# Optimization experiments

Measured on AMD Instinct MI355X. Metric: run time of the kernel, lower is better.

## Reference

```python
import jax, jax.numpy as jnp
import numpy as np

DIM = 1024
SCALE_DIM = 4
QK_DIM = DIM // SCALE_DIM  # 256
B, S = 4, 4096


def setup_inputs() -> dict:
    key = jax.random.key(0)
    ks = jax.random.split(key, 8)
    std = 1.0 / np.sqrt(DIM)  # keep activations O(1)
    return {
        "q": jax.random.normal(ks[0], (B, S, DIM), jnp.float32),
        "k": jax.random.normal(ks[1], (B, S, DIM), jnp.float32),
        "v": jax.random.normal(ks[2], (B, S, DIM), jnp.float32),
        "Wq": jax.random.normal(ks[3], (QK_DIM, DIM), jnp.float32) * std,
        "bq": jnp.zeros((QK_DIM,), jnp.float32),
        "Wk": jax.random.normal(ks[4], (QK_DIM, DIM), jnp.float32) * std,
        "bk": jnp.zeros((QK_DIM,), jnp.float32),
        "Wv": jax.random.normal(ks[5], (DIM, DIM), jnp.float32) * std,
        "bv": jnp.zeros((DIM,), jnp.float32),
    }


def reference(q, k, v, Wq, bq, Wk, bk, Wv, bv):
    scale = jnp.asarray(np.sqrt(QK_DIM), q.dtype)
    qp = jnp.einsum("bsd,ed->bse", q, Wq) + bq  # [B,S,QK_DIM]
    kp = jnp.einsum("bsd,ed->bse", k, Wk) + bk  # [B,S,QK_DIM]
    vp = jnp.einsum("bsd,ed->bse", v, Wv) + bv  # [B,S,DIM]
    z = jnp.einsum("bqe,bke->bqk", qp, kp)      # [B,S,S]
    z = jax.nn.sigmoid(z / scale)
    return jnp.einsum("bqk,bkd->bqd", z, vp)     # [B,S,DIM]
```

## Files before the change

### kernel.cpp

```cpp
#include <hip/hip_runtime.h>
#include <cstdint>
#include <cstddef>


typedef __bf16 bf16;
typedef __bf16 v8bf __attribute__((ext_vector_type(8)));
typedef __bf16 v4bf __attribute__((ext_vector_type(4)));
typedef float  v16f __attribute__((ext_vector_type(16)));

#define DIMV  1024
#define QKD   256
#define BATCH 4
#define SEQ   4096

#define TM 128
#define TN 128
#define BK 32

__global__ __launch_bounds__(256) void cast_f32_bf16(const float* __restrict__ in,
                                                     bf16* __restrict__ out, int n4) {
  int i = blockIdx.x * 256 + threadIdx.x;
  if (i >= n4) return;
  const float4 v = reinterpret_cast<const float4*>(in)[i];
  v4bf o;
  o[0] = (bf16)v.x; o[1] = (bf16)v.y; o[2] = (bf16)v.z; o[3] = (bf16)v.w;
  reinterpret_cast<v4bf*>(out)[i] = o;
}

__device__ __forceinline__ void gload_lds16(const void* g, void* l) {
  __builtin_amdgcn_global_load_lds((const __attribute__((address_space(1))) void*)g,
                                   (__attribute__((address_space(3))) void*)l,
                                   16, 0, 0);
}

template <int MODE>
__global__ __launch_bounds__(256) void gemm_nt(
    const bf16* __restrict__ A, long As_z,
    const bf16* __restrict__ B, long Bs_z,
    const float* __restrict__ bias0, const float* __restrict__ bias1,
    void* __restrict__ Cv, long Cs_z,
    int K, int lda, int ldb, int ldc) {
  __shared__ __align__(16) bf16 As[TM * BK];
  __shared__ __align__(16) bf16 Bs[TN * BK];
  const int tid  = threadIdx.x;
  const int wave = tid >> 6;
  const int lane = tid & 63;
  const int zb   = blockIdx.z;
  A = A + (size_t)zb * As_z;
  B = B + (size_t)zb * Bs_z;
  const float* bias = (MODE == 0 && zb) ? bias1 : bias0;

  const int row0 = blockIdx.x * TM;
  const int col0 = blockIdx.y * TN;
  const int wm = (wave & 1) * 64;
  const int wn = (wave >> 1) * 64;
  const int l31  = lane & 31;
  const int half = lane >> 5;

  v16f acc[2][2] = {};

  const char* gA = (const char*)A;
  const char* gB = (const char*)B;
  const size_t sA = (size_t)lda * 2;
  const size_t sB = (size_t)ldb * 2;

  const int row_s = tid >> 2;
  const int qg    = (tid & 3) ^ ((row_s >> 1) & 3);
  const int kb    = qg * 16;
  char* ldsA = (char*)As + wave * 1024;
  char* ldsB = (char*)Bs + wave * 1024;

  const char* pa0 = gA + (size_t)(row0 + row_s) * sA + kb;
  const char* pa1 = gA + (size_t)(row0 + row_s + 64) * sA + kb;
  const char* pb0 = gB + (size_t)(col0 + row_s) * sB + kb;
  const char* pb1 = gB + (size_t)(col0 + row_s + 64) * sB + kb;

  const int swz  = (lane >> 1) & 3;
  const int off0 = (half ^ swz) * 8;
  const int off1 = off0 ^ 16;
  const int raA0 = (wm + l31) * BK,      raA1 = (wm + 32 + l31) * BK;
  const int raB0 = (wn + l31) * BK,      raB1 = (wn + 32 + l31) * BK;

  const int kIters = K / BK;
  for (int kt = 0; kt < kIters; ++kt) {
    gload_lds16(pa0, ldsA);
    gload_lds16(pa1, ldsA + 4096);
    gload_lds16(pb0, ldsB);
    gload_lds16(pb1, ldsB + 4096);
    pa0 += BK * 2; pa1 += BK * 2; pb0 += BK * 2; pb1 += BK * 2;
    __syncthreads();

    v8bf a[2][2], b[2][2];
    a[0][0] = *(const v8bf*)&As[raA0 + off0];
    a[0][1] = *(const v8bf*)&As[raA0 + off1];
    a[1][0] = *(const v8bf*)&As[raA1 + off0];
    a[1][1] = *(const v8bf*)&As[raA1 + off1];
    b[0][0] = *(const v8bf*)&Bs[raB0 + off0];
    b[0][1] = *(const v8bf*)&Bs[raB0 + off1];
    b[1][0] = *(const v8bf*)&Bs[raB1 + off0];
    b[1][1] = *(const v8bf*)&Bs[raB1 + off1];
#pragma unroll
    for (int kk = 0; kk < 2; ++kk)
#pragma unroll
      for (int i = 0; i < 2; ++i)
#pragma unroll
        for (int j = 0; j < 2; ++j)
          acc[i][j] = __builtin_amdgcn_mfma_f32_32x32x16_bf16(a[i][kk], b[j][kk], acc[i][j], 0, 0, 0);
    __syncthreads();
  }

#pragma unroll
  for (int i = 0; i < 2; ++i) {
    const int rb = row0 + wm + i * 32 + 4 * half;
#pragma unroll
    for (int j = 0; j < 2; ++j) {
      const int gcol = col0 + wn + j * 32 + l31;
      float badd = 0.f;
      if (MODE == 0 || MODE == 1) badd = bias[gcol];
      if (MODE == 1) {
        const int b = rb >> 12;
        bf16* cb = &((bf16*)Cv)[((size_t)(b * DIMV + gcol)) * SEQ];
        const int s0 = rb & 4095;
#pragma unroll
        for (int blk = 0; blk < 4; ++blk) {
          v4bf o;
#pragma unroll
          for (int rr = 0; rr < 4; ++rr) o[rr] = (bf16)(acc[i][j][4 * blk + rr] + badd);
          *(v4bf*)&cb[s0 + 8 * blk] = o;
        }
      } else {
#pragma unroll
        for (int blk = 0; blk < 4; ++blk)
#pragma unroll
          for (int rr = 0; rr < 4; ++rr) {
            const int grow = rb + 8 * blk + rr;
            float v = acc[i][j][4 * blk + rr];
            if (MODE == 0) {
              ((bf16*)Cv)[(size_t)zb * Cs_z + (size_t)grow * ldc + gcol] = (bf16)(v + badd);
            } else if (MODE == 2) {
              v = 1.f / (1.f + __expf(v * -0.0625f));
              ((bf16*)Cv)[(size_t)zb * Cs_z + (size_t)grow * ldc + gcol] = (bf16)v;
            } else {
              ((float*)Cv)[(size_t)zb * Cs_z + (size_t)grow * ldc + gcol] = v;
            }
          }
      }
    }
  }
}

extern "C" void kernel_launch(void* const* d_in, const int* in_sizes, int n_in,
                              void* d_out, int out_size, void* d_ws, size_t ws_size,
                              hipStream_t stream) {
  const float* q  = (const float*)d_in[0];
  const float* k  = (const float*)d_in[1];
  const float* v  = (const float*)d_in[2];
  const float* Wq = (const float*)d_in[3];
  const float* bq = (const float*)d_in[4];
  const float* Wk = (const float*)d_in[5];
  const float* bk = (const float*)d_in[6];
  const float* Wv = (const float*)d_in[7];
  const float* bv = (const float*)d_in[8];
  float* out = (float*)d_out;

  const size_t MB = 1024 * 1024;
  char* ws = (char*)d_ws;

  int g;
  size_t zcap;
  if (ws_size >= 188 * MB)      { g = 4; zcap = 128 * MB; }
  else if (ws_size >= 121 * MB) { g = 2; zcap = 64 * MB; }
  else                          { g = 1; zcap = 64 * MB; }

  bf16 *castA, *castB, *zbuf, *Wq16, *Wk16, *Wv16, *qp16, *kp16, *vpT;
  if (g >= 2) {
    castA = (bf16*)ws;
    castB = (bf16*)(ws + 32 * MB);
    zbuf  = (bf16*)ws;
    char* p = ws + zcap;
    Wq16 = (bf16*)p;             p += 524288;
    Wk16 = (bf16*)p;             p += 524288;
    Wv16 = (bf16*)p;             p += 2097152;
    qp16 = (bf16*)p;             p += 8388608;
    kp16 = (bf16*)p;             p += 8388608;
    vpT  = (bf16*)p;
  } else {
    castA = (bf16*)ws;
    zbuf  = castA;
    char* p = ws + 32 * MB;
    Wq16 = (bf16*)p;             p += 524288;
    Wk16 = (bf16*)p;             p += 524288;
    Wv16 = (bf16*)p;             p += 2097152;
    qp16 = (bf16*)p;             p += 8388608;
    kp16 = (bf16*)p;             p += 8388608;
    vpT  = (bf16*)p;
    castB = vpT;
  }

  const int NQKV = BATCH * SEQ * DIMV;

  auto cast = [&](const float* src, bf16* dst, int n) {
    int n4 = n / 4;
    cast_f32_bf16<<<dim3((n4 + 255) / 256), dim3(256), 0, stream>>>(src, dst, n4);
  };

  cast(Wq, Wq16, QKD * DIMV);
  cast(Wk, Wk16, QKD * DIMV);
  cast(Wv, Wv16, DIMV * DIMV);
  cast(q, castA, NQKV);
  cast(k, castB, NQKV);

  gemm_nt<0><<<dim3(BATCH * SEQ / TM, QKD / TN, 2), dim3(256), 0, stream>>>(
      castA, (long)(castB - castA), Wq16, (long)(QKD * DIMV), bq, bk,
      qp16, (long)(kp16 - qp16), DIMV, DIMV, DIMV, QKD);

  cast(v, castA, NQKV);
  gemm_nt<1><<<dim3(BATCH * SEQ / TM, DIMV / TN, 1), dim3(256), 0, stream>>>(
      castA, 0L, Wv16, 0L, bv, nullptr,
      vpT, 0L, DIMV, DIMV, DIMV, 0);

  const long zstride = (long)SEQ * SEQ;
  for (int ig = 0; ig < BATCH / g; ++ig) {
    const size_t b0 = (size_t)ig * g;
    gemm_nt<2><<<dim3(SEQ / TM, SEQ / TN, g), dim3(256), 0, stream>>>(
        qp16 + b0 * SEQ * QKD, (long)(SEQ * QKD),
        kp16 + b0 * SEQ * QKD, (long)(SEQ * QKD),
        nullptr, nullptr, zbuf, zstride, QKD, QKD, QKD, SEQ);
    gemm_nt<3><<<dim3(SEQ / TM, DIMV / TN, g), dim3(256), 0, stream>>>(
        zbuf, zstride, vpT + b0 * DIMV * SEQ, (long)(DIMV * SEQ),
        nullptr, nullptr, out + b0 * SEQ * DIMV, (long)(SEQ * DIMV),
        SEQ, SEQ, SEQ, DIMV);
  }
}
```

Baseline: 547.2 us.

## Add 256x256-tile 8-wave double-buffered GEMM for V-proj, scores and output

Adds a new NT GEMM kernel with 256x256 tiles, 512 threads (8 waves), BK=64 and two LDS buffers of 128 KB in total. Global-to-LDS prefetch of the next K-slice is interleaved with 16x16x32 MFMA quarters using explicit barriers, waitcnt and setprio. It replaces the 128x128 kernel for the V projection, the sigmoid score GEMM and the final Z·V GEMM. The aim is more reuse per loaded byte and hiding load latency behind compute, at the cost of higher LDS and register use, which limits occupancy, and hand-tuned synchronisation that is fragile.

```diff
diff --git a/kernel.cpp b/kernel.cpp
--- a/kernel.cpp
+++ b/kernel.cpp
@@ -7,6 +7,7 @@
 typedef __bf16 v8bf __attribute__((ext_vector_type(8)));
 typedef __bf16 v4bf __attribute__((ext_vector_type(4)));
 typedef float  v16f __attribute__((ext_vector_type(16)));
+typedef float  v4f  __attribute__((ext_vector_type(4)));
 
 #define DIMV  1024
 #define QKD   256
@@ -147,6 +148,176 @@
       }
     }
   }
+}
+
+#define FENCE() asm volatile("" ::: "memory")
+#define BAR8()  do { FENCE(); __builtin_amdgcn_s_barrier(); FENCE(); } while (0)
+#define WAIT_LGKM0() asm volatile("s_waitcnt lgkmcnt(0)" ::: "memory")
+#define WAIT_VM6()   asm volatile("s_waitcnt vmcnt(6)" ::: "memory")
+#define WAIT_VM0()   asm volatile("s_waitcnt vmcnt(0)" ::: "memory")
+
+template <int MODE>
+__global__ __launch_bounds__(512, 2) void gemm_nt8(
+    const bf16* __restrict__ A, long As_z,
+    const bf16* __restrict__ B, long Bs_z,
+    const float* __restrict__ bias0,
+    void* __restrict__ Cv, long Cs_z,
+    int K, int lda, int ldb, int ldc) {
+  __shared__ __align__(16) bf16 lds[2][4][8192];
+  char* ldsBase = (char*)&lds[0][0][0];
+  const int tid = threadIdx.x;
+  const int w   = tid >> 6;
+  const int l   = tid & 63;
+  const int zb  = blockIdx.z;
+  A += (size_t)zb * As_z;
+  B += (size_t)zb * Bs_z;
+
+  const int row0 = blockIdx.x * 256;
+  const int col0 = blockIdx.y * 256;
+  const int wmi  = w >> 2;
+  const int wni  = w & 3;
+  const int l4 = l & 15, lh = l >> 4;
+
+  const int rsub = l >> 3;
+  const int cg   = (l & 7) ^ rsub;
+  const size_t sA = (size_t)lda * 2, sB = (size_t)ldb * 2;
+  const size_t sA64 = sA * 64, sB64 = sB * 64;
+  const char* pA0 = (const char*)A + (size_t)(row0 +       w * 8 + rsub) * sA + cg * 16;
+  const char* pA1 = (const char*)A + (size_t)(row0 + 128 + w * 8 + rsub) * sA + cg * 16;
+  const char* pB0 = (const char*)B + (size_t)(col0 +       w * 8 + rsub) * sB + cg * 16;
+  const char* pB1 = (const char*)B + (size_t)(col0 + 128 + w * 8 + rsub) * sB + cg * 16;
+  const int wq = w * 1024;
+
+  const int off0 = l4 * 128 + ((lh ^ (l & 7)) << 4);
+  const int off1 = off0 ^ 64;
+
+  v4f acc[8][4] = {};
+
+#define STAGE_K(ptr, sec, d, s64)                                   \
+  do {                                                              \
+    char* _lb = ldsBase + (d) * 65536 + (sec) * 16384 + wq;         \
+    gload_lds16(ptr, _lb);                                          \
+    gload_lds16((ptr) + (s64), _lb + 8192);                         \
+    (ptr) += 128;                                                   \
+  } while (0)
+
+#define READ_A(MOFF)                                                         \
+  _Pragma("unroll") for (int mm = 0; mm < 4; ++mm) {                         \
+    a_[mm][0] = *(const v8bf*)(aB + ((MOFF) + mm) * 2048 + off0);            \
+    a_[mm][1] = *(const v8bf*)(aB + ((MOFF) + mm) * 2048 + off1);            \
+  }
+#define READ_B()                                                             \
+  _Pragma("unroll") for (int nn = 0; nn < 4; ++nn) {                         \
+    b_[nn][0] = *(const v8bf*)(bB + nn * 2048 + off0);                       \
+    b_[nn][1] = *(const v8bf*)(bB + nn * 2048 + off1);                       \
+  }
+#define MFMA_Q(M0, N0)                                                       \
+  _Pragma("unroll") for (int mm = 0; mm < 4; ++mm)                           \
+  _Pragma("unroll") for (int nn = 0; nn < 2; ++nn)                           \
+  _Pragma("unroll") for (int kk = 0; kk < 2; ++kk)                           \
+    acc[(M0) + mm][(N0) + nn] = __builtin_amdgcn_mfma_f32_16x16x32_bf16(     \
+        a_[mm][kk], b_[(N0) + nn][kk], acc[(M0) + mm][(N0) + nn], 0, 0, 0);
+
+  const int nt = K >> 6;
+
+  STAGE_K(pB0, 2, 0, sB64);
+  STAGE_K(pB1, 3, 0, sB64);
+  STAGE_K(pA0, 0, 0, sA64);
+  STAGE_K(pA1, 1, 0, sA64);
+  STAGE_K(pB0, 2, 1, sB64);
+  STAGE_K(pB1, 3, 1, sB64);
+  STAGE_K(pA0, 0, 1, sA64);
+  WAIT_VM6();
+  BAR8();
+
+  v8bf a_[4][2], b_[4][2];
+
+  for (int t = 0; t < nt - 1; ++t) {
+    const int d  = t & 1;
+    const int dn = d ^ 1;
+    const char* aB = ldsBase + d * 65536 + wmi * 16384;
+    const char* bB = ldsBase + d * 65536 + 32768 + (wni >> 1) * 16384 + (wni & 1) * 8192;
+    const bool pf = (t < nt - 2);
+    READ_A(0);
+    READ_B();
+    STAGE_K(pA1, 1, dn, sA64);
+    BAR8();
+    WAIT_LGKM0();
+    __builtin_amdgcn_s_setprio(1);
+    MFMA_Q(0, 0);
+    __builtin_amdgcn_s_setprio(0);
+    BAR8();
+    if (pf) STAGE_K(pB0, 2, d, sB64);
+    BAR8();
+    WAIT_LGKM0();
+    __builtin_amdgcn_s_setprio(1);
+    MFMA_Q(0, 2);
+    __builtin_amdgcn_s_setprio(0);
+    BAR8();
+    READ_A(4);
+    if (pf) STAGE_K(pB1, 3, d, sB64);
+    BAR8();
+    WAIT_LGKM0();
+    __builtin_amdgcn_s_setprio(1);
+    MFMA_Q(4, 0);
+    __builtin_amdgcn_s_setprio(0);
+    BAR8();
+    if (pf) STAGE_K(pA0, 0, d, sA64);
+    BAR8();
+    WAIT_LGKM0();
+    __builtin_amdgcn_s_setprio(1);
+    MFMA_Q(4, 2);
+    __builtin_amdgcn_s_setprio(0);
+    if (pf) WAIT_VM6(); else WAIT_VM0();
+    BAR8();
+  }
+  {
+    const int d = (nt - 1) & 1;
+    const char* aB = ldsBase + d * 65536 + wmi * 16384;
+    const char* bB = ldsBase + d * 65536 + 32768 + (wni >> 1) * 16384 + (wni & 1) * 8192;
+    READ_A(0);
+    READ_B();
+    MFMA_Q(0, 0);
+    MFMA_Q(0, 2);
+    READ_A(4);
+    MFMA_Q(4, 0);
+    MFMA_Q(4, 2);
+  }
+
+  const int rbase = row0 + wmi * 128 + 4 * lh;
+#pragma unroll
+  for (int mm = 0; mm < 8; ++mm) {
+    const int rb = rbase + mm * 16;
+#pragma unroll
+    for (int nn = 0; nn < 4; ++nn) {
+      const int gcol = col0 + wni * 64 + nn * 16 + l4;
+      if (MODE == 1) {
+        const int b = rb >> 12;
+        bf16* cb = &((bf16*)Cv)[((size_t)(b * DIMV + gcol)) * SEQ];
+        const int s0 = rb & 4095;
+        const float badd = bias0[gcol];
+        v4bf o;
+#pragma unroll
+        for (int rr = 0; rr < 4; ++rr) o[rr] = (bf16)(acc[mm][nn][rr] + badd);
+        *(v4bf*)&cb[s0] = o;
+      } else if (MODE == 2) {
+#pragma unroll
+        for (int rr = 0; rr < 4; ++rr) {
+          float v = acc[mm][nn][rr];
+          v = 1.f / (1.f + __expf(v * -0.0625f));
+          ((bf16*)Cv)[(size_t)zb * Cs_z + (size_t)(rb + rr) * ldc + gcol] = (bf16)v;
+        }
+      } else {
+#pragma unroll
+        for (int rr = 0; rr < 4; ++rr)
+          ((float*)Cv)[(size_t)zb * Cs_z + (size_t)(rb + rr) * ldc + gcol] = acc[mm][nn][rr];
+      }
+    }
+  }
+#undef STAGE_K
+#undef READ_A
+#undef READ_B
+#undef MFMA_Q
 }
 
 extern "C" void kernel_launch(void* const* d_in, const int* in_sizes, int n_in,
@@ -215,20 +386,20 @@
       qp16, (long)(kp16 - qp16), DIMV, DIMV, DIMV, QKD);
 
   cast(v, castA, NQKV);
-  gemm_nt<1><<<dim3(BATCH * SEQ / TM, DIMV / TN, 1), dim3(256), 0, stream>>>(
-      castA, 0L, Wv16, 0L, bv, nullptr,
+  gemm_nt8<1><<<dim3(BATCH * SEQ / 256, DIMV / 256, 1), dim3(512), 0, stream>>>(
+      castA, 0L, Wv16, 0L, bv,
       vpT, 0L, DIMV, DIMV, DIMV, 0);
 
   const long zstride = (long)SEQ * SEQ;
   for (int ig = 0; ig < BATCH / g; ++ig) {
     const size_t b0 = (size_t)ig * g;
-    gemm_nt<2><<<dim3(SEQ / TM, SEQ / TN, g), dim3(256), 0, stream>>>(
+    gemm_nt8<2><<<dim3(SEQ / 256, SEQ / 256, g), dim3(512), 0, stream>>>(
         qp16 + b0 * SEQ * QKD, (long)(SEQ * QKD),
         kp16 + b0 * SEQ * QKD, (long)(SEQ * QKD),
-        nullptr, nullptr, zbuf, zstride, QKD, QKD, QKD, SEQ);
-    gemm_nt<3><<<dim3(SEQ / TM, DIMV / TN, g), dim3(256), 0, stream>>>(
+        nullptr, zbuf, zstride, QKD, QKD, QKD, SEQ);
+    gemm_nt8<3><<<dim3(SEQ / 256, DIMV / 256, g), dim3(512), 0, stream>>>(
         zbuf, zstride, vpT + b0 * DIMV * SEQ, (long)(DIMV * SEQ),
-        nullptr, nullptr, out + b0 * SEQ * DIMV, (long)(SEQ * DIMV),
+        nullptr, out + b0 * SEQ * DIMV, (long)(SEQ * DIMV),
         SEQ, SEQ, SEQ, DIMV);
   }
 }
```

New measurement: 473.2 us. -13.5%, faster.
